# Performance work log

Measured on AMD Instinct MI355X. Metric: run time of the kernel, lower is better.

The kernel has to match this reference:

```python
import jax, jax.numpy as jnp
import numpy as np

N_NODES = 100000
D_IN = 128
D_OUT = 128
N_EDGES = 50000
EDGE_SIZE = 16  # nodes per hyperedge (assumed unique within an edge)


def setup_inputs() -> dict:
    key = jax.random.key(0)
    ks = jax.random.split(key, 8)
    # hypergraph in flat membership (CSR-like) form
    member_nodes = jax.random.randint(ks[0], (N_EDGES * EDGE_SIZE,), 0, N_NODES)
    edge_ids = jnp.repeat(jnp.arange(N_EDGES), EDGE_SIZE)
    H = jax.random.normal(ks[1], (N_NODES, D_IN), dtype=jnp.float32)
    input_weight = jax.random.uniform(ks[2], (N_NODES, 2), dtype=jnp.float32)
    std = 1.0 / np.sqrt(D_OUT)
    W = jax.random.uniform(ks[3], (D_IN, D_OUT), minval=-std, maxval=std, dtype=jnp.float32)
    bias = jax.random.uniform(ks[4], (D_OUT,), minval=-std, maxval=std, dtype=jnp.float32)

    def lin(k, fan_in, fan_out):
        b = 1.0 / np.sqrt(fan_in)
        k1, k2 = jax.random.split(k)
        w = jax.random.uniform(k1, (fan_in, fan_out), minval=-b, maxval=b, dtype=jnp.float32)
        bb = jax.random.uniform(k2, (fan_out,), minval=-b, maxval=b, dtype=jnp.float32)
        return w, bb

    fc1_w, fc1_b = lin(ks[5], 2, 10)
    fc2_w, fc2_b = lin(ks[6], 10, 5)
    fc3_w, fc3_b = lin(ks[7], 5, 1)
    return {
        "member_nodes": member_nodes, "edge_ids": edge_ids,
        "H": H, "input_weight": input_weight,
        "W": W, "bias": bias,
        "fc1_w": fc1_w, "fc1_b": fc1_b,
        "fc2_w": fc2_w, "fc2_b": fc2_b,
        "fc3_w": fc3_w, "fc3_b": fc3_b,
    }


def reference(member_nodes, edge_ids, H, input_weight, W, bias,
              fc1_w, fc1_b, fc2_w, fc2_b, fc3_w, fc3_b):
    # Weight_net (eval mode -> dropout is identity): per-node scalar weight in (0,1)
    h1 = jax.nn.relu(input_weight @ fc1_w + fc1_b)
    h2 = jax.nn.relu(h1 @ fc2_w + fc2_b)
    W2 = jax.nn.sigmoid(h2 @ fc3_w + fc3_b)  # [N, 1]

    # signal_shift_hypergraph_: per-edge weighted sum, broadcast, scatter-add
    HW2 = H * W2                                   # [N, d]
    gathered = HW2[member_nodes]                   # [M, d]
    edge_sum = jax.ops.segment_sum(gathered, edge_ids, num_segments=N_EDGES)   # [E, d]
    edge_size = jax.ops.segment_sum(jnp.ones((member_nodes.shape[0],), H.dtype),
                                    edge_ids, num_segments=N_EDGES)            # [E]
    contrib = (edge_sum[edge_ids] - H[member_nodes]) / (edge_size[edge_ids] - 1.0)[:, None]
    new_signal = H + jax.ops.segment_sum(contrib, member_nodes, num_segments=N_NODES)

    # row-normalize (1/rowsum with inf -> 0)
    rowsum = new_signal.sum(axis=1)
    r_inv = jnp.where(rowsum != 0, 1.0 / rowsum, 0.0)
    AH = new_signal * r_inv[:, None]

    return AH @ W + bias
```

## Files before the change

kernel.cpp:

```cpp
#include <hip/hip_runtime.h>
#include <math.h>

#define EDGE_SZ 16
#define CAP 32
#define BIN_CAP 2560

typedef __attribute__((ext_vector_type(8))) short bf16x8;
typedef __attribute__((ext_vector_type(4))) float f32x4;

__device__ __forceinline__ unsigned short f2bf(float x) {
    unsigned u = __builtin_bit_cast(unsigned, x);
    unsigned r = (u + 0x7fff + ((u >> 16) & 1)) >> 16;
    return (unsigned short)r;
}
__device__ __forceinline__ unsigned pack2bf(float lo, float hi) {
    return ((unsigned)f2bf(hi) << 16) | (unsigned)f2bf(lo);
}
__device__ __forceinline__ float bf_lo(unsigned u) {
    return __builtin_bit_cast(float, u << 16);
}
__device__ __forceinline__ float bf_hi(unsigned u) {
    return __builtin_bit_cast(float, u & 0xffff0000u);
}

__global__ __launch_bounds__(256) void init_kernel(
    const float* __restrict__ W, unsigned short* __restrict__ Wtg,
    int* __restrict__ binCursor, int nbins,
    unsigned* __restrict__ esbSent, float* __restrict__ SeSent,
    const float* __restrict__ iw,
    const float* __restrict__ fc1_w, const float* __restrict__ fc1_b,
    const float* __restrict__ fc2_w, const float* __restrict__ fc2_b,
    const float* __restrict__ fc3_w, const float* __restrict__ fc3_b,
    float* __restrict__ w2v, int n)
{
    int i = blockIdx.x * blockDim.x + threadIdx.x;
    if (i < nbins) binCursor[i] = 0;
    if (i < 64) esbSent[i] = 0u;
    if (i == 64) *SeSent = 0.f;
    if (i < 16384) {
        int nn = i >> 7, k = i & 127;
        Wtg[i] = f2bf(W[k * 128 + nn]);
    }
    if (i < n) {
        float xx = iw[i * 2 + 0], xy = iw[i * 2 + 1];
        float h1[10];
#pragma unroll
        for (int j = 0; j < 10; ++j) {
            float v = xx * fc1_w[j] + xy * fc1_w[10 + j] + fc1_b[j];
            h1[j] = v > 0.f ? v : 0.f;
        }
        float h2[5];
#pragma unroll
        for (int j = 0; j < 5; ++j) {
            float v = fc2_b[j];
#pragma unroll
            for (int k = 0; k < 10; ++k) v += h1[k] * fc2_w[k * 5 + j];
            h2[j] = v > 0.f ? v : 0.f;
        }
        float z = fc3_b[0];
#pragma unroll
        for (int j = 0; j < 5; ++j) z += h2[j] * fc3_w[j];
        w2v[i] = 1.f / (1.f + expf(-z));
    }
}

__global__ __launch_bounds__(256) void bin_prep_kernel(
    const int* __restrict__ mn, int* __restrict__ binCursor,
    unsigned* __restrict__ stage, int m,
    const float* __restrict__ H, const float* __restrict__ w2v,
    unsigned* __restrict__ Hwb, float* __restrict__ Hs, float* __restrict__ Hws,
    int n, int bin_blocks)
{
    __shared__ int hist[512];
    __shared__ int base[512];
    int t = threadIdx.x;
    if ((int)blockIdx.x < bin_blocks) {
        for (int i = t; i < 512; i += 256) hist[i] = 0;
        __syncthreads();
        int start = blockIdx.x * 2048;
        int nodev[8], loff[8];
#pragma unroll
        for (int j = 0; j < 8; ++j) {
            int i = start + j * 256 + t;
            nodev[j] = (i < m) ? mn[i] : -1;
            loff[j] = (nodev[j] >= 0) ? atomicAdd(&hist[nodev[j] >> 8], 1) : 0;
        }
        __syncthreads();
        for (int b = t; b < 512; b += 256)
            base[b] = (hist[b] > 0) ? atomicAdd(&binCursor[b], hist[b]) : 0;
        __syncthreads();
#pragma unroll
        for (int j = 0; j < 8; ++j) {
            if (nodev[j] >= 0) {
                int b = nodev[j] >> 8;
                int pos = base[b] + loff[j];
                int i = start + j * 256 + t;
                if (pos < BIN_CAP)
                    stage[b * BIN_CAP + pos] =
                        ((unsigned)(i >> 4) << 8) | (unsigned)(nodev[j] & 255);
            }
        }
        return;
    }
    int wave = __builtin_amdgcn_readfirstlane(
        ((int)blockIdx.x - bin_blocks) * (blockDim.x >> 6) + (t >> 6));
    int lane = t & 63;
    if (wave >= n) return;
    float w2 = w2v[wave];
    float2 h = ((const float2*)H)[wave * 64 + lane];
    Hwb[wave * 64 + lane] = pack2bf(h.x * w2, h.y * w2);
    float part = h.x + h.y;
#pragma unroll
    for (int off = 32; off >= 1; off >>= 1) part += __shfl_xor(part, off, 64);
    if (lane == 0) { Hs[wave] = part; Hws[wave] = part * w2; }
}

__global__ __launch_bounds__(256) void bucket_edge_kernel(
    const unsigned* __restrict__ stage, const int* __restrict__ binCursor,
    unsigned short* __restrict__ bucket, int* __restrict__ cursor,
    const int* __restrict__ mn, const unsigned* __restrict__ Hwb,
    const float* __restrict__ Hws, unsigned* __restrict__ esb,
    float* __restrict__ Se, int n, int nbins, int E)
{
    __shared__ __align__(16) unsigned short lb[256 * CAP];
    __shared__ int lc[256];
    int t = threadIdx.x;
    if ((int)blockIdx.x < nbins) {
        int b = blockIdx.x;
        unsigned sent = (unsigned)E * 0x10001u;
        for (int i = t; i < 4096; i += 256) ((unsigned*)lb)[i] = sent;
        lc[t] = 0;
        __syncthreads();
        int cnt = binCursor[b]; if (cnt > BIN_CAP) cnt = BIN_CAP;
        for (int i = t; i < cnt; i += 256) {
            unsigned u = stage[b * BIN_CAP + i];
            int nloc = u & 255;
            int e = u >> 8;
            int p = atomicAdd(&lc[nloc], 1);
            if (p < CAP) lb[nloc * CAP + p] = (unsigned short)e;
        }
        __syncthreads();
        int nbase = b << 8;
        for (int i = t; i < 1024; i += 256) {
            int nloc = i >> 2;
            int node = nbase + nloc;
            if (node < n)
                ((uint4*)bucket)[(size_t)node * 4 + (i & 3)] = ((const uint4*)lb)[i];
        }
        int node = nbase + t;
        if (node < n) cursor[node] = lc[t];
        return;
    }
    int pair = __builtin_amdgcn_readfirstlane(
        ((int)blockIdx.x - nbins) * (blockDim.x >> 6) + (t >> 6));
    int lane = t & 63;
    int e0 = pair * 2;
    if (e0 >= E) return;
    int e1 = e0 + 1;
    int n0[EDGE_SZ], n1[EDGE_SZ];
#pragma unroll
    for (int mm = 0; mm < EDGE_SZ; ++mm) n0[mm] = mn[e0 * EDGE_SZ + mm];
#pragma unroll
    for (int mm = 0; mm < EDGE_SZ; ++mm) n1[mm] = mn[e1 * EDGE_SZ + mm];
    unsigned u0[EDGE_SZ], u1[EDGE_SZ];
#pragma unroll
    for (int mm = 0; mm < EDGE_SZ; ++mm) u0[mm] = Hwb[n0[mm] * 64 + lane];
#pragma unroll
    for (int mm = 0; mm < EDGE_SZ; ++mm) u1[mm] = Hwb[n1[mm] * 64 + lane];
    float se0 = 0.f, se1 = 0.f;
#pragma unroll
    for (int mm = 0; mm < EDGE_SZ; ++mm) { se0 += Hws[n0[mm]]; se1 += Hws[n1[mm]]; }
    float ax0 = 0.f, ay0 = 0.f, ax1 = 0.f, ay1 = 0.f;
#pragma unroll
    for (int mm = 0; mm < EDGE_SZ; ++mm) {
        ax0 += bf_lo(u0[mm]); ay0 += bf_hi(u0[mm]);
        ax1 += bf_lo(u1[mm]); ay1 += bf_hi(u1[mm]);
    }
    esb[e0 * 64 + lane] = pack2bf(ax0, ay0);
    esb[e1 * 64 + lane] = pack2bf(ax1, ay1);
    if (lane == 0) { Se[e0] = se0; Se[e1] = se1; }
}

__global__ __launch_bounds__(256) void node_update_kernel(
    const float* __restrict__ H, const unsigned* __restrict__ esb,
    const float* __restrict__ Hs, const float* __restrict__ Se,
    const int* __restrict__ cursor, const unsigned short* __restrict__ bucket,
    unsigned* __restrict__ AHb, int n, int E)
{
    int grp = __builtin_amdgcn_readfirstlane(
        blockIdx.x * (blockDim.x >> 6) + (threadIdx.x >> 6));
    int lane = threadIdx.x & 63;
    int base = grp * 4;
    if (base >= n) return;
    float2 h[4];
    int d[4];
    const unsigned* bp[4];
    float ax[4], ay[4], ss[4];
    int dm = 0;
#pragma unroll
    for (int q = 0; q < 4; ++q) {
        int nq = base + q; if (nq >= n) nq = n - 1;
        h[q] = ((const float2*)H)[nq * 64 + lane];
        int dq = cursor[nq]; if (dq > CAP) dq = CAP;
        if (base + q >= n) dq = 0;
        d[q] = dq;
        if (dq > dm) dm = dq;
        bp[q] = (const unsigned*)(bucket + (size_t)nq * CAP);
        ax[q] = 0.f; ay[q] = 0.f; ss[q] = 0.f;
    }
    for (int k0 = 0; k0 < dm; k0 += 8) {
        unsigned ev[4][8];
#pragma unroll
        for (int q = 0; q < 4; ++q)
#pragma unroll
            for (int j = 0; j < 8; ++j) {
                unsigned dw = bp[q][(k0 >> 1) + (j >> 1)];
                ev[q][j] = (j & 1) ? (dw >> 16) : (dw & 0xffffu);
            }
        unsigned v[4][8];
#pragma unroll
        for (int q = 0; q < 4; ++q)
#pragma unroll
            for (int j = 0; j < 8; ++j) v[q][j] = esb[ev[q][j] * 64 + lane];
        float s[4][8];
#pragma unroll
        for (int q = 0; q < 4; ++q)
#pragma unroll
            for (int j = 0; j < 8; ++j) s[q][j] = Se[ev[q][j]];
#pragma unroll
        for (int q = 0; q < 4; ++q)
#pragma unroll
            for (int j = 0; j < 8; ++j) {
                ax[q] += bf_lo(v[q][j]);
                ay[q] += bf_hi(v[q][j]);
                ss[q] += s[q][j];
            }
    }
    const float inv15 = 1.f / 15.f;
#pragma unroll
    for (int q = 0; q < 4; ++q) {
        if (base + q >= n) break;
        int nq = base + q;
        float sc = 1.f - (float)d[q] * inv15;
        float nx = h[q].x * sc + ax[q] * inv15;
        float ny = h[q].y * sc + ay[q] * inv15;
        float st = Hs[nq] * sc + ss[q] * inv15;
        float ri = (st != 0.f) ? 1.f / st : 0.f;
        AHb[nq * 64 + lane] = pack2bf(nx * ri, ny * ri);
    }
}

#define WT_LD 136
__global__ __launch_bounds__(256) void gemm_kernel(
    const unsigned short* __restrict__ AHb, const unsigned short* __restrict__ Wtg,
    const float* __restrict__ bias, float* __restrict__ out, int M)
{
    __shared__ short Wt[128 * WT_LD];
    int t = threadIdx.x;
    for (int i = t; i < 8192; i += 256) {
        unsigned dw = ((const unsigned*)Wtg)[i];
        int n = i >> 6, k2 = i & 63;
        *(unsigned*)&Wt[n * WT_LD + k2 * 2] = dw;
    }
    __syncthreads();

    int lane = t & 63;
    int m16 = lane & 15;
    int quad = lane >> 4;
    int wrow0 = blockIdx.x * 64 + (t >> 6) * 16;

    int arow = wrow0 + m16;
    if (arow >= M) arow = M - 1;

    f32x4 acc[8] = {};
#pragma unroll
    for (int kc = 0; kc < 4; ++kc) {
        int k0 = kc * 32;
        bf16x8 a = *(const bf16x8*)&AHb[arow * 128 + k0 + quad * 8];
#pragma unroll
        for (int ct = 0; ct < 8; ++ct) {
            bf16x8 b = *(const bf16x8*)&Wt[(ct * 16 + m16) * WT_LD + k0 + quad * 8];
            acc[ct] = __builtin_amdgcn_mfma_f32_16x16x32_bf16(a, b, acc[ct], 0, 0, 0);
        }
    }

#pragma unroll
    for (int ct = 0; ct < 8; ++ct) {
        float bv = bias[ct * 16 + m16];
#pragma unroll
        for (int r = 0; r < 4; ++r) {
            int row = wrow0 + quad * 4 + r;
            if (row < M)
                out[row * 128 + ct * 16 + m16] = acc[ct][r] + bv;
        }
    }
}

extern "C" void kernel_launch(void* const* d_in, const int* in_sizes, int n_in,
                              void* d_out, int out_size, void* d_ws, size_t ws_size,
                              hipStream_t stream)
{
    const int*   mn   = (const int*)d_in[0];
    const float* H    = (const float*)d_in[2];
    const float* iw   = (const float*)d_in[3];
    const float* W    = (const float*)d_in[4];
    const float* bias = (const float*)d_in[5];
    const float* fc1w = (const float*)d_in[6];
    const float* fc1b = (const float*)d_in[7];
    const float* fc2w = (const float*)d_in[8];
    const float* fc2b = (const float*)d_in[9];
    const float* fc3w = (const float*)d_in[10];
    const float* fc3b = (const float*)d_in[11];
    float* out = (float*)d_out;

    const int M = in_sizes[0];
    const int E = M / EDGE_SZ;
    const int N = in_sizes[2] / 128;
    const int nbins = (N + 255) >> 8;

    char* ws = (char*)d_ws;
    size_t off = 0;
    auto alloc = [&](size_t bytes) -> char* {
        char* p = ws + off;
        off = (off + bytes + 15) & ~(size_t)15;
        return p;
    };
    unsigned*       Hwb    = (unsigned*)alloc((size_t)N * 64 * 4);
    float*          Hs     = (float*)alloc((size_t)N * 4);
    float*          Hws    = (float*)alloc((size_t)N * 4);
    unsigned*       esb    = (unsigned*)alloc((size_t)(E + 1) * 64 * 4);
    float*          Se     = (float*)alloc((size_t)(E + 1) * 4);
    unsigned*       AHb    = (unsigned*)alloc((size_t)N * 64 * 4);
    int*            cursor = (int*)alloc((size_t)N * 4);
    unsigned short* bucket = (unsigned short*)alloc((size_t)N * CAP * 2);
    unsigned short* Wtg    = (unsigned short*)alloc((size_t)128 * 128 * 2);
    int*            binCur = (int*)alloc((size_t)nbins * 4);
    unsigned*       stage  = (unsigned*)alloc((size_t)nbins * BIN_CAP * 4);
    float*          w2v    = (float*)alloc((size_t)N * 4);
    (void)ws_size;

    const int bin_blocks  = (M + 2047) / 2048;
    const int prep_blocks = (N + 3) / 4;
    const int edge_blocks = (E / 2 + 3) / 4;

    init_kernel<<<(N + 255) / 256, 256, 0, stream>>>(
        W, Wtg, binCur, nbins, esb + (size_t)E * 64, Se + E,
        iw, fc1w, fc1b, fc2w, fc2b, fc3w, fc3b, w2v, N);
    bin_prep_kernel<<<bin_blocks + prep_blocks, 256, 0, stream>>>(
        mn, binCur, stage, M, H, w2v, Hwb, Hs, Hws, N, bin_blocks);
    bucket_edge_kernel<<<nbins + edge_blocks, 256, 0, stream>>>(
        stage, binCur, bucket, cursor, mn, Hwb, Hws, esb, Se, N, nbins, E);
    node_update_kernel<<<((N + 3) / 4 + 3) / 4, 256, 0, stream>>>(
        H, esb, Hs, Se, cursor, bucket, AHb, N, E);
    gemm_kernel<<<(N + 63) / 64, 256, 0, stream>>>(
        (const unsigned short*)AHb, Wtg, bias, out, N);
}
```

Baseline: 235.6 us.

## Fuse node update with output GEMM via shared-memory AH tile

Merges the node-update and GEMM kernels into one 512-thread kernel. Each block computes 64 normalized node rows into an LDS tile, then runs MFMA against W read directly from global memory. This removes the global round trip of the bf16 AH intermediate and one kernel launch. In exchange, W is no longer staged in LDS, and there is a block-wide sync between the gather phase and the GEMM phase.

```diff
diff --git a/kernel.cpp b/kernel.cpp
--- a/kernel.cpp
+++ b/kernel.cpp
@@ -4,6 +4,7 @@
 #define EDGE_SZ 16
 #define CAP 32
 #define BIN_CAP 2560
+#define AH_LD 136
 
 typedef __attribute__((ext_vector_type(8))) short bf16x8;
 typedef __attribute__((ext_vector_type(4))) float f32x4;
@@ -181,117 +182,107 @@
     if (lane == 0) { Se[e0] = se0; Se[e1] = se1; }
 }
 
-__global__ __launch_bounds__(256) void node_update_kernel(
+__global__ __launch_bounds__(512) void node_gemm_kernel(
     const float* __restrict__ H, const unsigned* __restrict__ esb,
     const float* __restrict__ Hs, const float* __restrict__ Se,
     const int* __restrict__ cursor, const unsigned short* __restrict__ bucket,
-    unsigned* __restrict__ AHb, int n, int E)
-{
-    int grp = __builtin_amdgcn_readfirstlane(
-        blockIdx.x * (blockDim.x >> 6) + (threadIdx.x >> 6));
-    int lane = threadIdx.x & 63;
-    int base = grp * 4;
-    if (base >= n) return;
-    float2 h[4];
-    int d[4];
-    const unsigned* bp[4];
-    float ax[4], ay[4], ss[4];
-    int dm = 0;
-#pragma unroll
-    for (int q = 0; q < 4; ++q) {
-        int nq = base + q; if (nq >= n) nq = n - 1;
-        h[q] = ((const float2*)H)[nq * 64 + lane];
-        int dq = cursor[nq]; if (dq > CAP) dq = CAP;
-        if (base + q >= n) dq = 0;
-        d[q] = dq;
-        if (dq > dm) dm = dq;
-        bp[q] = (const unsigned*)(bucket + (size_t)nq * CAP);
-        ax[q] = 0.f; ay[q] = 0.f; ss[q] = 0.f;
-    }
-    for (int k0 = 0; k0 < dm; k0 += 8) {
-        unsigned ev[4][8];
-#pragma unroll
-        for (int q = 0; q < 4; ++q)
-#pragma unroll
-            for (int j = 0; j < 8; ++j) {
-                unsigned dw = bp[q][(k0 >> 1) + (j >> 1)];
-                ev[q][j] = (j & 1) ? (dw >> 16) : (dw & 0xffffu);
-            }
-        unsigned v[4][8];
-#pragma unroll
-        for (int q = 0; q < 4; ++q)
-#pragma unroll
-            for (int j = 0; j < 8; ++j) v[q][j] = esb[ev[q][j] * 64 + lane];
-        float s[4][8];
-#pragma unroll
-        for (int q = 0; q < 4; ++q)
-#pragma unroll
-            for (int j = 0; j < 8; ++j) s[q][j] = Se[ev[q][j]];
-#pragma unroll
-        for (int q = 0; q < 4; ++q)
-#pragma unroll
-            for (int j = 0; j < 8; ++j) {
-                ax[q] += bf_lo(v[q][j]);
-                ay[q] += bf_hi(v[q][j]);
-                ss[q] += s[q][j];
-            }
-    }
+    const unsigned short* __restrict__ Wtg, const float* __restrict__ bias,
+    float* __restrict__ out, int n, int E)
+{
+    __shared__ __align__(16) short AH[64 * AH_LD];
+    int t = threadIdx.x;
+    int w = t >> 6;
+    int lane = t & 63;
     const float inv15 = 1.f / 15.f;
-#pragma unroll
-    for (int q = 0; q < 4; ++q) {
-        if (base + q >= n) break;
-        int nq = base + q;
-        float sc = 1.f - (float)d[q] * inv15;
-        float nx = h[q].x * sc + ax[q] * inv15;
-        float ny = h[q].y * sc + ay[q] * inv15;
-        float st = Hs[nq] * sc + ss[q] * inv15;
-        float ri = (st != 0.f) ? 1.f / st : 0.f;
-        AHb[nq * 64 + lane] = pack2bf(nx * ri, ny * ri);
-    }
-}
-
-#define WT_LD 136
-__global__ __launch_bounds__(256) void gemm_kernel(
-    const unsigned short* __restrict__ AHb, const unsigned short* __restrict__ Wtg,
-    const float* __restrict__ bias, float* __restrict__ out, int M)
-{
-    __shared__ short Wt[128 * WT_LD];
-    int t = threadIdx.x;
-    for (int i = t; i < 8192; i += 256) {
-        unsigned dw = ((const unsigned*)Wtg)[i];
-        int n = i >> 6, k2 = i & 63;
-        *(unsigned*)&Wt[n * WT_LD + k2 * 2] = dw;
+    int nodeBase = blockIdx.x * 64 + w * 8;
+
+    for (int g = 0; g < 2; ++g) {
+        int base = nodeBase + g * 4;
+        float2 h[4];
+        int d[4];
+        const unsigned* bp[4];
+        float ax[4], ay[4], ss[4];
+        int dm = 0;
+#pragma unroll
+        for (int q = 0; q < 4; ++q) {
+            int nq = base + q; if (nq >= n) nq = n - 1;
+            h[q] = ((const float2*)H)[nq * 64 + lane];
+            int dq = cursor[nq]; if (dq > CAP) dq = CAP;
+            if (base + q >= n) dq = 0;
+            d[q] = dq;
+            if (dq > dm) dm = dq;
+            bp[q] = (const unsigned*)(bucket + (size_t)nq * CAP);
+            ax[q] = 0.f; ay[q] = 0.f; ss[q] = 0.f;
+        }
+        for (int k0 = 0; k0 < dm; k0 += 8) {
+            unsigned ev[4][8];
+#pragma unroll
+            for (int q = 0; q < 4; ++q)
+#pragma unroll
+                for (int j = 0; j < 8; ++j) {
+                    unsigned dw = bp[q][(k0 >> 1) + (j >> 1)];
+                    ev[q][j] = (j & 1) ? (dw >> 16) : (dw & 0xffffu);
+                }
+            unsigned v[4][8];
+#pragma unroll
+            for (int q = 0; q < 4; ++q)
+#pragma unroll
+                for (int j = 0; j < 8; ++j) v[q][j] = esb[ev[q][j] * 64 + lane];
+            float s[4][8];
+#pragma unroll
+            for (int q = 0; q < 4; ++q)
+#pragma unroll
+                for (int j = 0; j < 8; ++j) s[q][j] = Se[ev[q][j]];
+#pragma unroll
+            for (int q = 0; q < 4; ++q)
+#pragma unroll
+                for (int j = 0; j < 8; ++j) {
+                    ax[q] += bf_lo(v[q][j]);
+                    ay[q] += bf_hi(v[q][j]);
+                    ss[q] += s[q][j];
+                }
+        }
+#pragma unroll
+        for (int q = 0; q < 4; ++q) {
+            int nq = base + q; if (nq >= n) nq = n - 1;
+            float sc = 1.f - (float)d[q] * inv15;
+            float nx = h[q].x * sc + ax[q] * inv15;
+            float ny = h[q].y * sc + ay[q] * inv15;
+            float st = Hs[nq] * sc + ss[q] * inv15;
+            float ri = (st != 0.f) ? 1.f / st : 0.f;
+            *(unsigned*)&AH[(w * 8 + g * 4 + q) * AH_LD + lane * 2] =
+                pack2bf(nx * ri, ny * ri);
+        }
     }
     __syncthreads();
 
-    int lane = t & 63;
     int m16 = lane & 15;
     int quad = lane >> 4;
-    int wrow0 = blockIdx.x * 64 + (t >> 6) * 16;
-
-    int arow = wrow0 + m16;
-    if (arow >= M) arow = M - 1;
-
-    f32x4 acc[8] = {};
+    int rt = w >> 1;
+    int ch = w & 1;
+    int rowl = rt * 16 + m16;
+    f32x4 acc[4] = {};
 #pragma unroll
     for (int kc = 0; kc < 4; ++kc) {
         int k0 = kc * 32;
-        bf16x8 a = *(const bf16x8*)&AHb[arow * 128 + k0 + quad * 8];
-#pragma unroll
-        for (int ct = 0; ct < 8; ++ct) {
-            bf16x8 b = *(const bf16x8*)&Wt[(ct * 16 + m16) * WT_LD + k0 + quad * 8];
+        bf16x8 a = *(const bf16x8*)&AH[rowl * AH_LD + k0 + quad * 8];
+#pragma unroll
+        for (int ct = 0; ct < 4; ++ct) {
+            int col = ch * 64 + ct * 16 + m16;
+            bf16x8 b = *(const bf16x8*)&Wtg[col * 128 + k0 + quad * 8];
             acc[ct] = __builtin_amdgcn_mfma_f32_16x16x32_bf16(a, b, acc[ct], 0, 0, 0);
         }
     }
-
-#pragma unroll
-    for (int ct = 0; ct < 8; ++ct) {
-        float bv = bias[ct * 16 + m16];
+    int wrow0 = blockIdx.x * 64 + rt * 16;
+#pragma unroll
+    for (int ct = 0; ct < 4; ++ct) {
+        int col = ch * 64 + ct * 16 + m16;
+        float bv = bias[col];
 #pragma unroll
         for (int r = 0; r < 4; ++r) {
             int row = wrow0 + quad * 4 + r;
-            if (row < M)
-                out[row * 128 + ct * 16 + m16] = acc[ct][r] + bv;
+            if (row < n)
+                out[row * 128 + col] = acc[ct][r] + bv;
         }
     }
 }
@@ -330,7 +321,6 @@
     float*          Hws    = (float*)alloc((size_t)N * 4);
     unsigned*       esb    = (unsigned*)alloc((size_t)(E + 1) * 64 * 4);
     float*          Se     = (float*)alloc((size_t)(E + 1) * 4);
-    unsigned*       AHb    = (unsigned*)alloc((size_t)N * 64 * 4);
     int*            cursor = (int*)alloc((size_t)N * 4);
     unsigned short* bucket = (unsigned short*)alloc((size_t)N * CAP * 2);
     unsigned short* Wtg    = (unsigned short*)alloc((size_t)128 * 128 * 2);
@@ -350,8 +340,6 @@
         mn, binCur, stage, M, H, w2v, Hwb, Hs, Hws, N, bin_blocks);
     bucket_edge_kernel<<<nbins + edge_blocks, 256, 0, stream>>>(
         stage, binCur, bucket, cursor, mn, Hwb, Hws, esb, Se, N, nbins, E);
-    node_update_kernel<<<((N + 3) / 4 + 3) / 4, 256, 0, stream>>>(
-        H, esb, Hs, Se, cursor, bucket, AHb, N, E);
-    gemm_kernel<<<(N + 63) / 64, 256, 0, stream>>>(
-        (const unsigned short*)AHb, Wtg, bias, out, N);
-}
+    node_gemm_kernel<<<(N + 63) / 64, 512, 0, stream>>>(
+        H, esb, Hs, Se, cursor, bucket, Wtg, bias, out, N, E);
+}
```

Result: slower. 283.5 us (+20.3%).
